# Kernel optimization log

Hardware: AMD Instinct MI355X
Metric: run time of the kernel (lower is better)

The kernel has to match this reference:

```python
import jax, jax.numpy as jnp
import numpy as np

N_NODES = 50000
N_EDGES = 800000
H = 128   # hidden_dim
E = 64    # edge_dim
LN_EPS = 1e-5


def _layer_norm(x, g, b):
    m = jnp.mean(x, axis=-1, keepdims=True)
    v = jnp.mean(jnp.square(x - m), axis=-1, keepdims=True)
    return (x - m) * jax.lax.rsqrt(v + LN_EPS) * g + b


def _gelu(x):
    return jax.nn.gelu(x, approximate=False)  # torch default exact GELU


def setup_inputs() -> dict:
    key = jax.random.key(0)
    ks = jax.random.split(key, 24)

    def lin(k, fin, fout):
        kw, kb = jax.random.split(k)
        s = 1.0 / np.sqrt(fin)
        W = jax.random.uniform(kw, (fin, fout), jnp.float32, -s, s)
        b = jax.random.uniform(kb, (fout,), jnp.float32, -s, s)
        return W, b

    inp = {}
    inp["x"] = jax.random.normal(ks[0], (N_NODES, H), jnp.float32)
    inp["edge_emb"] = jax.random.normal(ks[1], (N_EDGES, E), jnp.float32)
    inp["time_weight"] = jax.random.uniform(ks[2], (N_EDGES, 1), jnp.float32)
    inp["message_node_scale"] = jax.random.uniform(ks[3], (N_NODES, 1), jnp.float32)
    inp["ln1_g"] = jnp.ones((H,), jnp.float32)
    inp["ln1_b"] = jnp.zeros((H,), jnp.float32)
    inp["ln2_g"] = jnp.ones((H,), jnp.float32)
    inp["ln2_b"] = jnp.zeros((H,), jnp.float32)
    inp["selfW"], inp["selfb"] = lin(ks[4], H, H)
    inp["msgW1"], inp["msgb1"] = lin(ks[5], H + E, H)
    inp["msgW2"], inp["msgb2"] = lin(ks[6], H, H)
    inp["gateW1"], inp["gateb1"] = lin(ks[7], 2 * H + E, H)
    inp["gateW2"], inp["gateb2"] = lin(ks[8], H, 1)
    inp["aggW"], inp["aggb"] = lin(ks[9], H, H)
    inp["ffnW1"], inp["ffnb1"] = lin(ks[10], H, 2 * H)
    inp["ffnW2"], inp["ffnb2"] = lin(ks[11], 2 * H, H)
    inp["edge_src"] = jax.random.randint(ks[12], (N_EDGES,), 0, N_NODES, jnp.int32)
    inp["edge_dst"] = jax.random.randint(ks[13], (N_EDGES,), 0, N_NODES, jnp.int32)
    return inp


def reference(x, edge_emb, time_weight, message_node_scale,
              ln1_g, ln1_b, ln2_g, ln2_b,
              selfW, selfb, msgW1, msgb1, msgW2, msgb2,
              gateW1, gateb1, gateW2, gateb2,
              aggW, aggb, ffnW1, ffnb1, ffnW2, ffnb2,
              edge_src, edge_dst):
    n_nodes = x.shape[0]
    n_edges = edge_dst.shape[0]

    h = _layer_norm(x, ln1_g, ln1_b)
    hs = h[edge_src]  # [NE, H]
    hd = h[edge_dst]  # [NE, H]

    msg = _gelu(jnp.concatenate([hs, edge_emb], -1) @ msgW1 + msgb1) @ msgW2 + msgb2
    gate = jax.nn.sigmoid(
        _gelu(jnp.concatenate([hd, hs, edge_emb], -1) @ gateW1 + gateb1) @ gateW2 + gateb2)
    edge_repr = gate * msg
    edge_repr = edge_repr * time_weight
    edge_scale = 0.5 * (message_node_scale[edge_src] + message_node_scale[edge_dst])
    edge_repr = edge_repr * edge_scale

    agg = jax.ops.segment_sum(edge_repr, edge_dst, num_segments=n_nodes)
    deg = jax.ops.segment_sum(jnp.ones((n_edges, 1), x.dtype), edge_dst,
                              num_segments=n_nodes)
    agg = agg / jnp.maximum(deg, 1.0)

    update = (h @ selfW + selfb) + (agg @ aggW + aggb)
    out = x + update  # residual; dropout is identity at inference

    h2 = _layer_norm(out, ln2_g, ln2_b)
    ffn_update = _gelu(h2 @ ffnW1 + ffnb1) @ ffnW2 + ffnb2
    out = out + ffn_update
    return (out, edge_repr)
```

## Files before the change

### kernel.cpp

```cpp
#include <hip/hip_runtime.h>


typedef __attribute__((ext_vector_type(8))) short short8;
typedef __attribute__((ext_vector_type(4))) float f32x4;

#define NN 50000
#define NEDGE 800000

#define MFMA(a, b, c) __builtin_amdgcn_mfma_f32_16x16x32_bf16(a, b, c, 0, 0, 0)

__device__ __forceinline__ unsigned short f2bf(float f) {
  unsigned int u = __float_as_uint(f);
  u += 0x7fffu + ((u >> 16) & 1u);
  return (unsigned short)(u >> 16);
}
__device__ __forceinline__ float bf2f(unsigned short u) {
  return __uint_as_float((unsigned int)u << 16);
}
__device__ __forceinline__ unsigned int cvtpk(float a, float b) {
  unsigned int d;
  asm("v_cvt_pk_bf16_f32 %0, %1, %2" : "=v"(d) : "v"(a), "v"(b));
  return d;
}
__device__ __forceinline__ float geluf(float x) {
  const float t = x * fmaf(-0.1029437f, x * x, -2.3022211f);
  return x * __builtin_amdgcn_rcpf(1.0f + exp2f(t));
}
__device__ __forceinline__ short8 ld8(const unsigned short* p) {
  return *reinterpret_cast<const short8*>(p);
}
__device__ __forceinline__ int swz256(int row, int byteoff) {
  return row * 256 + (byteoff ^ ((row & 15) << 4));
}
__device__ __forceinline__ int swz128(int row, int byteoff) {
  return row * 128 + (byteoff ^ ((row & 7) << 4));
}

__device__ __forceinline__ void ln_frags(const float* __restrict__ rowp,
                                         const float* __restrict__ g,
                                         const float* __restrict__ b, int koff,
                                         short8 a[4]) {
  f32x4 v[8];
#pragma unroll
  for (int s = 0; s < 4; s++) {
    v[2 * s] = *reinterpret_cast<const f32x4*>(rowp + s * 32 + koff);
    v[2 * s + 1] = *reinterpret_cast<const f32x4*>(rowp + s * 32 + koff + 4);
  }
  float sm = 0.f;
#pragma unroll
  for (int i = 0; i < 8; i++) sm += v[i][0] + v[i][1] + v[i][2] + v[i][3];
  sm += __shfl_xor(sm, 16);
  sm += __shfl_xor(sm, 32);
  const float mean = sm * 0.0078125f;
  float sq = 0.f;
#pragma unroll
  for (int i = 0; i < 8; i++) {
#pragma unroll
    for (int t = 0; t < 4; t++) {
      const float d = v[i][t] - mean;
      sq += d * d;
    }
  }
  sq += __shfl_xor(sq, 16);
  sq += __shfl_xor(sq, 32);
  const float rs = rsqrtf(sq * 0.0078125f + 1e-5f);
#pragma unroll
  for (int s = 0; s < 4; s++) {
    const f32x4 glo = *reinterpret_cast<const f32x4*>(g + s * 32 + koff);
    const f32x4 ghi = *reinterpret_cast<const f32x4*>(g + s * 32 + koff + 4);
    const f32x4 blo = *reinterpret_cast<const f32x4*>(b + s * 32 + koff);
    const f32x4 bhi = *reinterpret_cast<const f32x4*>(b + s * 32 + koff + 4);
    float y[8];
#pragma unroll
    for (int t = 0; t < 4; t++) {
      y[t] = (v[2 * s][t] - mean) * rs * glo[t] + blo[t];
      y[4 + t] = (v[2 * s + 1][t] - mean) * rs * ghi[t] + bhi[t];
    }
    union { unsigned int u[4]; short8 s8; } pk;
    pk.u[0] = cvtpk(y[0], y[1]);
    pk.u[1] = cvtpk(y[2], y[3]);
    pk.u[2] = cvtpk(y[4], y[5]);
    pk.u[3] = cvtpk(y[6], y[7]);
    a[s] = pk.s8;
  }
}

__global__ __launch_bounds__(256) void prep_kernel(
    const float* __restrict__ selfW, const float* __restrict__ msgW1,
    const float* __restrict__ msgW2, const float* __restrict__ gateW1,
    const float* __restrict__ aggW, const float* __restrict__ ffnW1,
    const float* __restrict__ ffnW2, unsigned short* __restrict__ wts) {
  const int idx = blockIdx.x * 256 + threadIdx.x;
  if (idx < 16384) {
    int n = idx >> 7, k = idx & 127;
    wts[idx] = f2bf(selfW[k * 128 + n]);
  } else if (idx < 32768) {
    int l = idx - 16384, n = l >> 7, k = l & 127;
    wts[idx] = f2bf(aggW[k * 128 + n]);
  } else if (idx < 57344) {
    int l = idx - 32768, n = l / 192, k = l - n * 192;
    wts[idx] = f2bf(msgW1[k * 128 + n]);
  } else if (idx < 73728) {
    int l = idx - 57344, n = l >> 7, k = l & 127;
    wts[idx] = f2bf(msgW2[k * 128 + n]);
  } else if (idx < 114688) {
    int l = idx - 73728, n = l / 320, k = l - n * 320;
    wts[idx] = f2bf(gateW1[k * 128 + n]);
  } else if (idx < 147456) {
    int l = idx - 114688, n = l >> 7, k = l & 127;
    wts[idx] = f2bf(ffnW1[k * 256 + n]);
  } else if (idx < 180224) {
    int l = idx - 147456, n = l >> 8, k = l & 255;
    wts[idx] = f2bf(ffnW2[k * 128 + n]);
  }
}

__global__ __launch_bounds__(256) void node_pre_kernel(
    const float* __restrict__ x, const float* __restrict__ ln1g,
    const float* __restrict__ ln1b, const unsigned short* __restrict__ wts,
    unsigned short* __restrict__ pd, unsigned short* __restrict__ psm) {
  const int wid = threadIdx.x >> 6, lane = threadIdx.x & 63;
  const int q = lane >> 4, r16 = lane & 15, koff = q * 8;
  const int r0 = blockIdx.x * 64 + wid * 16;
  const int row = min(r0 + r16, NN - 1);
  const unsigned short* gateW1T = wts + 73728;
  const unsigned short* msgW1T = wts + 32768;
  short8 a[4];
  ln_frags(x + (size_t)row * 128, ln1g, ln1b, koff, a);
  f32x4 acc[3][8];
#pragma unroll
  for (int t = 0; t < 3; t++)
#pragma unroll
    for (int nt = 0; nt < 8; nt++) acc[t][nt] = (f32x4){0.f, 0.f, 0.f, 0.f};
#pragma unroll
  for (int s = 0; s < 4; s++) {
    const int k0 = s * 32 + koff;
#pragma unroll
    for (int nt = 0; nt < 8; nt++) {
      const int c = nt * 16 + r16;
      acc[0][nt] = MFMA(a[s], ld8(gateW1T + c * 320 + k0), acc[0][nt]);
      acc[1][nt] = MFMA(a[s], ld8(gateW1T + c * 320 + 128 + k0), acc[1][nt]);
      acc[2][nt] = MFMA(a[s], ld8(msgW1T + c * 192 + k0), acc[2][nt]);
    }
  }
#pragma unroll
  for (int j = 0; j < 4; j++) {
    const int gr = r0 + q * 4 + j;
    if (gr < NN) {
#pragma unroll
      for (int nt = 0; nt < 8; nt++) {
        const int c = nt * 16 + r16;
        pd[(size_t)gr * 128 + c] = f2bf(acc[0][nt][j]);
        psm[(size_t)gr * 256 + c] = f2bf(acc[1][nt][j]);
        psm[(size_t)gr * 256 + 128 + c] = f2bf(acc[2][nt][j]);
      }
    }
  }
}

__global__ __launch_bounds__(256) void count_kernel(
    const int* __restrict__ edst, int* __restrict__ cnt) {
  const int e = blockIdx.x * 256 + threadIdx.x;
  atomicAdd(&cnt[edst[e]], 1);
}

__global__ __launch_bounds__(256) void scan_sums_kernel(
    const int* __restrict__ cnt, int* __restrict__ bsum) {
  const int gi = blockIdx.x * 256 + threadIdx.x;
  int v = (gi < NN) ? cnt[gi] : 0;
#pragma unroll
  for (int m = 1; m < 64; m <<= 1) v += __shfl_xor(v, m);
  __shared__ int wsum[4];
  if ((threadIdx.x & 63) == 0) wsum[threadIdx.x >> 6] = v;
  __syncthreads();
  if (threadIdx.x == 0)
    bsum[blockIdx.x] = wsum[0] + wsum[1] + wsum[2] + wsum[3];
}

__global__ __launch_bounds__(256) void scan_offsets_kernel(
    const int* __restrict__ bsum, int* __restrict__ boff, int nb) {
  __shared__ int tmp[256];
  const int tid = threadIdx.x;
  const int v = (tid < nb) ? bsum[tid] : 0;
  tmp[tid] = v;
  __syncthreads();
#pragma unroll
  for (int d = 1; d < 256; d <<= 1) {
    const int t = (tid >= d) ? tmp[tid - d] : 0;
    __syncthreads();
    tmp[tid] += t;
    __syncthreads();
  }
  if (tid < nb) boff[tid] = tmp[tid] - v;
}

__global__ __launch_bounds__(256) void scan_final_kernel(
    const int* __restrict__ cnt, const int* __restrict__ boff,
    int* __restrict__ row_start, int* __restrict__ cursor) {
  const int tid = threadIdx.x, lane = tid & 63, wid = tid >> 6;
  const int gi = blockIdx.x * 256 + tid;
  const int val = (gi < NN) ? cnt[gi] : 0;
  int v = val;
#pragma unroll
  for (int d = 1; d < 64; d <<= 1) {
    const int t = __shfl_up(v, d);
    if (lane >= d) v += t;
  }
  __shared__ int wsum[4];
  if (lane == 63) wsum[wid] = v;
  __syncthreads();
  int woff = 0;
  for (int w = 0; w < wid; ++w) woff += wsum[w];
  const int excl = (v - val) + woff + boff[blockIdx.x];
  if (gi < NN) {
    row_start[gi] = excl;
    cursor[gi] = excl;
  }
  if (gi == NN - 1) row_start[NN] = excl + val;
}

__global__ __launch_bounds__(256) void scatter_kernel(
    const int* __restrict__ esrc, const int* __restrict__ edst,
    const float* __restrict__ tw, const float* __restrict__ mns,
    int* __restrict__ cursor, int4* __restrict__ etab) {
  const int e = blockIdx.x * 256 + threadIdx.x;
  const int si = esrc[e];
  const int di = edst[e];
  const int pos = atomicAdd(&cursor[di], 1);
  const float sc = tw[e] * 0.5f * (mns[si] + mns[di]);
  int4 v;
  v.x = e;
  v.y = si;
  v.z = di;
  v.w = __float_as_int(sc);
  etab[pos] = v;
}

__global__ __launch_bounds__(512, 6) void edge_kernel(
    const float* __restrict__ emb, const int4* __restrict__ etab,
    const unsigned short* __restrict__ pd,
    const unsigned short* __restrict__ psm,
    const unsigned short* __restrict__ wts, const float* __restrict__ msgb1,
    const float* __restrict__ msgb2, const float* __restrict__ gateb1,
    const float* __restrict__ gateW2, const float* __restrict__ gateb2v,
    float* __restrict__ erout, float* __restrict__ aggf) {
  __shared__ __align__(16) char buf[64 * 256 + 64 * 256 + 64 * 128];
  __shared__ float p_s[4][64];
  __shared__ float G_s[64];
  __shared__ float sc_s[64];
  __shared__ int di_s[64], eidx_s[64];

  char* pgp = buf;
  char* pmp = buf + 16384;
  char* embp = buf + 32768;
  float* xbuf = (float*)buf;

  const int tid = threadIdx.x;
  const int lane = tid & 63;
  const int wid = tid >> 6;
  const int q = lane >> 4;
  const int r16 = lane & 15;
  const int koff = q * 8;
  const int mg = wid >> 2;
  const int ng = wid & 3;
  const int e0 = blockIdx.x * 64;

  const unsigned short* gateW1T = wts + 73728;
  const unsigned short* msgW1T = wts + 32768;
  const unsigned short* msgW2T = wts + 57344;

  if (tid < 64) {
    const int4 et = etab[e0 + tid];
    eidx_s[tid] = et.x;
    di_s[tid] = et.z;
    sc_s[tid] = __int_as_float(et.w);
  }

#pragma unroll
  for (int r = 0; r < 2; r++) {
    const int unit = tid + 512 * r;
    const int row = unit >> 4;
    const int c = unit & 15;
    const int4 et = etab[e0 + row];
    const int si = et.y, di = et.z;
    const short8 vd = ld8(pd + (size_t)di * 128 + c * 8);
    const short8 vs = ld8(psm + (size_t)si * 256 + c * 8);
    union { unsigned int u[4]; short8 s; } pk;
#pragma unroll
    for (int h = 0; h < 4; h++) {
      const float f0 =
          bf2f((unsigned short)vd[2 * h]) + bf2f((unsigned short)vs[2 * h]);
      const float f1 = bf2f((unsigned short)vd[2 * h + 1]) +
                       bf2f((unsigned short)vs[2 * h + 1]);
      pk.u[h] = cvtpk(f0, f1);
    }
    *reinterpret_cast<short8*>(pgp + swz256(row, c * 16)) = pk.s;
    *reinterpret_cast<short8*>(pmp + swz256(row, c * 16)) =
        ld8(psm + (size_t)si * 256 + 128 + c * 8);
  }
  if (tid < 256) {
    const int row = tid >> 2, c4 = tid & 3;
    const int e = etab[e0 + row].x;
#pragma unroll
    for (int i = 0; i < 4; i++) {
      const f32x4 v =
          *reinterpret_cast<const f32x4*>(emb + (size_t)e * 64 + c4 * 16 + i * 4);
      uint2 w;
      w.x = cvtpk(v[0], v[1]);
      w.y = cvtpk(v[2], v[3]);
      *reinterpret_cast<uint2*>(embp + swz128(row, c4 * 32 + i * 8)) = w;
    }
  }
  __syncthreads();

  int cc[2];
  float g1[2], w2[2], b1m[2], b2m[2];
#pragma unroll
  for (int i = 0; i < 2; i++) {
    cc[i] = ng * 32 + i * 16 + r16;
    g1[i] = gateb1[cc[i]];
    w2[i] = gateW2[cc[i]];
    b1m[i] = msgb1[cc[i]];
    b2m[i] = msgb2[cc[i]];
  }

  f32x4 accg[2][2], acc1[2][2];
#pragma unroll
  for (int m = 0; m < 2; m++)
#pragma unroll
    for (int i = 0; i < 2; i++) {
      accg[m][i] = (f32x4){0.f, 0.f, 0.f, 0.f};
      acc1[m][i] = (f32x4){0.f, 0.f, 0.f, 0.f};
    }
#pragma unroll
  for (int s = 0; s < 2; s++) {
    const int k0 = s * 32 + koff;
    short8 a[2];
#pragma unroll
    for (int m = 0; m < 2; m++)
      a[m] = *reinterpret_cast<const short8*>(
          embp + swz128(mg * 32 + m * 16 + r16, k0 * 2));
#pragma unroll
    for (int i = 0; i < 2; i++) {
      const short8 bg = ld8(gateW1T + cc[i] * 320 + 256 + k0);
      const short8 bm = ld8(msgW1T + cc[i] * 192 + 128 + k0);
#pragma unroll
      for (int m = 0; m < 2; m++) {
        accg[m][i] = MFMA(a[m], bg, accg[m][i]);
        acc1[m][i] = MFMA(a[m], bm, acc1[m][i]);
      }
    }
  }

#pragma unroll
  for (int m = 0; m < 2; m++) {
#pragma unroll
    for (int j = 0; j < 4; j++) {
      const int row = mg * 32 + m * 16 + q * 4 + j;
      float v = 0.f;
#pragma unroll
      for (int i = 0; i < 2; i++) {
        const float pg = bf2f(*reinterpret_cast<const unsigned short*>(
            pgp + swz256(row, cc[i] * 2)));
        v += geluf(accg[m][i][j] + pg + g1[i]) * w2[i];
      }
      v += __shfl_xor(v, 1);
      v += __shfl_xor(v, 2);
      v += __shfl_xor(v, 4);
      v += __shfl_xor(v, 8);
      if (r16 == 0) p_s[ng][row] = v;
    }
  }

#pragma unroll
  for (int m = 0; m < 2; m++) {
#pragma unroll
    for (int i = 0; i < 2; i++) {
#pragma unroll
      for (int j = 0; j < 4; j++) {
        const int row = mg * 32 + m * 16 + q * 4 + j;
        unsigned short* ap =
            reinterpret_cast<unsigned short*>(pmp + swz256(row, cc[i] * 2));
        const float pm = bf2f(*ap);
        *ap = f2bf(geluf(acc1[m][i][j] + pm + b1m[i]));
      }
    }
  }
  __syncthreads();

  if (tid < 64) {
    const float p = gateb2v[0] + p_s[0][tid] + p_s[1][tid] + p_s[2][tid] +
                    p_s[3][tid];
    G_s[tid] =
        sc_s[tid] * __builtin_amdgcn_rcpf(1.f + exp2f(-1.4426950f * p));
  }

  f32x4 acc2[2][2];
#pragma unroll
  for (int m = 0; m < 2; m++)
#pragma unroll
    for (int i = 0; i < 2; i++) acc2[m][i] = (f32x4){0.f, 0.f, 0.f, 0.f};
#pragma unroll
  for (int s = 0; s < 4; s++) {
    const int k0 = s * 32 + koff;
    short8 a[2];
#pragma unroll
    for (int m = 0; m < 2; m++)
      a[m] = *reinterpret_cast<const short8*>(
          pmp + swz256(mg * 32 + m * 16 + r16, k0 * 2));
#pragma unroll
    for (int i = 0; i < 2; i++) {
      const short8 b = ld8(msgW2T + cc[i] * 128 + k0);
#pragma unroll
      for (int m = 0; m < 2; m++) acc2[m][i] = MFMA(a[m], b, acc2[m][i]);
    }
  }
  __syncthreads();

#pragma unroll
  for (int m = 0; m < 2; m++)
#pragma unroll
    for (int i = 0; i < 2; i++)
#pragma unroll
      for (int j = 0; j < 4; j++) {
        const int row = mg * 32 + m * 16 + q * 4 + j;
        xbuf[row * 132 + cc[i]] = G_s[row] * (acc2[m][i][j] + b2m[i]);
      }
  __syncthreads();

#pragma unroll
  for (int u = 0; u < 4; u++) {
    const int unit = tid + u * 512;
    const int r = unit >> 5;
    const int f4 = unit & 31;
    const f32x4 val = *reinterpret_cast<const f32x4*>(&xbuf[r * 132 + f4 * 4]);
    *reinterpret_cast<f32x4*>(erout + (size_t)eidx_s[r] * 128 + f4 * 4) = val;
  }

  {
    const int col = tid & 127;
    const int qt = tid >> 7;
    const int rbeg = qt * 16, rend = rbeg + 16;
    float acc = 0.f;
    int prev = di_s[rbeg];
    for (int r = rbeg; r < rend; ++r) {
      const int d = di_s[r];
      if (d != prev) {
        atomicAdd(&aggf[(size_t)prev * 128 + col], acc);
        acc = 0.f;
        prev = d;
      }
      acc += xbuf[r * 132 + col];
    }
    atomicAdd(&aggf[(size_t)prev * 128 + col], acc);
  }
}

__global__ __launch_bounds__(256) void node1_kernel(
    const float* __restrict__ x, const float* __restrict__ ln1g,
    const float* __restrict__ ln1b, const float* __restrict__ aggf,
    const int* __restrict__ row_start, const unsigned short* __restrict__ wts,
    const float* __restrict__ selfb, const float* __restrict__ aggb,
    float* __restrict__ out1) {
  const int wid = threadIdx.x >> 6, lane = threadIdx.x & 63;
  const int q = lane >> 4, r16 = lane & 15, koff = q * 8;
  const int r0 = blockIdx.x * 64 + wid * 16;
  const int row = min(r0 + r16, NN - 1);
  const float inv = __builtin_amdgcn_rcpf(
      fmaxf((float)(row_start[row + 1] - row_start[row]), 1.0f));
  const unsigned short* selfWT = wts;
  const unsigned short* aggWT = wts + 16384;
  short8 a1[4];
  ln_frags(x + (size_t)row * 128, ln1g, ln1b, koff, a1);
  f32x4 acc[8];
#pragma unroll
  for (int nt = 0; nt < 8; nt++) acc[nt] = (f32x4){0.f, 0.f, 0.f, 0.f};
#pragma unroll
  for (int s = 0; s < 4; s++) {
    const int k0 = s * 32 + koff;
    const float* ap = aggf + (size_t)row * 128 + k0;
    const f32x4 f0 = *reinterpret_cast<const f32x4*>(ap);
    const f32x4 f1 = *reinterpret_cast<const f32x4*>(ap + 4);
    union { unsigned int u[4]; short8 s; } pk;
    pk.u[0] = cvtpk(f0[0] * inv, f0[1] * inv);
    pk.u[1] = cvtpk(f0[2] * inv, f0[3] * inv);
    pk.u[2] = cvtpk(f1[0] * inv, f1[1] * inv);
    pk.u[3] = cvtpk(f1[2] * inv, f1[3] * inv);
#pragma unroll
    for (int nt = 0; nt < 8; nt++) {
      acc[nt] = MFMA(a1[s], ld8(selfWT + (nt * 16 + r16) * 128 + k0), acc[nt]);
      acc[nt] = MFMA(pk.s, ld8(aggWT + (nt * 16 + r16) * 128 + k0), acc[nt]);
    }
  }
#pragma unroll
  for (int j = 0; j < 4; j++) {
    const int gr = r0 + q * 4 + j;
    if (gr < NN) {
#pragma unroll
      for (int nt = 0; nt < 8; nt++) {
        const int c = r16 + 16 * nt;
        out1[(size_t)gr * 128 + c] =
            x[(size_t)gr * 128 + c] + acc[nt][j] + selfb[c] + aggb[c];
      }
    }
  }
}

__global__ __launch_bounds__(256) void ffn_kernel(
    const float* __restrict__ out1, const float* __restrict__ ln2g,
    const float* __restrict__ ln2b, const unsigned short* __restrict__ wts,
    const float* __restrict__ b1, const float* __restrict__ b2,
    float* __restrict__ outp) {
  __shared__ unsigned short ts[4][16 * 264];
  const int wid = threadIdx.x >> 6, lane = threadIdx.x & 63;
  const int q = lane >> 4, r16 = lane & 15, koff = q * 8;
  const int r0 = blockIdx.x * 64 + wid * 16;
  const int row = min(r0 + r16, NN - 1);
  const unsigned short* W1T = wts + 114688;
  const unsigned short* W2T = wts + 147456;
  short8 a[4];
  ln_frags(out1 + (size_t)row * 128, ln2g, ln2b, koff, a);
  f32x4 acc1[16];
#pragma unroll
  for (int nt = 0; nt < 16; nt++) acc1[nt] = (f32x4){0.f, 0.f, 0.f, 0.f};
#pragma unroll
  for (int s = 0; s < 4; s++) {
    const int k0 = s * 32 + koff;
#pragma unroll
    for (int nt = 0; nt < 16; nt++)
      acc1[nt] = MFMA(a[s], ld8(W1T + (nt * 16 + r16) * 128 + k0), acc1[nt]);
  }
  unsigned short* tw_ = ts[wid];
#pragma unroll
  for (int nt = 0; nt < 16; nt++) {
    const int c = r16 + 16 * nt;
    const float bb = b1[c];
#pragma unroll
    for (int j = 0; j < 4; j++)
      tw_[(q * 4 + j) * 264 + c] = f2bf(geluf(acc1[nt][j] + bb));
  }
  __syncthreads();
  f32x4 acc2[8];
#pragma unroll
  for (int nt = 0; nt < 8; nt++) acc2[nt] = (f32x4){0.f, 0.f, 0.f, 0.f};
#pragma unroll
  for (int s = 0; s < 8; s++) {
    const int k0 = s * 32 + koff;
    const short8 av = *reinterpret_cast<const short8*>(tw_ + r16 * 264 + k0);
#pragma unroll
    for (int nt = 0; nt < 8; nt++)
      acc2[nt] = MFMA(av, ld8(W2T + (nt * 16 + r16) * 256 + k0), acc2[nt]);
  }
#pragma unroll
  for (int j = 0; j < 4; j++) {
    const int gr = r0 + q * 4 + j;
    if (gr < NN) {
#pragma unroll
      for (int nt = 0; nt < 8; nt++) {
        const int c = r16 + 16 * nt;
        outp[(size_t)gr * 128 + c] =
            out1[(size_t)gr * 128 + c] + acc2[nt][j] + b2[c];
      }
    }
  }
}

extern "C" void kernel_launch(void* const* d_in, const int* in_sizes, int n_in,
                              void* d_out, int out_size, void* d_ws,
                              size_t ws_size, hipStream_t stream) {
  (void)in_sizes; (void)n_in; (void)out_size; (void)ws_size;
  const float* x = (const float*)d_in[0];
  const float* emb = (const float*)d_in[1];
  const float* tw = (const float*)d_in[2];
  const float* mns = (const float*)d_in[3];
  const float* ln1g = (const float*)d_in[4];
  const float* ln1b = (const float*)d_in[5];
  const float* ln2g = (const float*)d_in[6];
  const float* ln2b = (const float*)d_in[7];
  const float* selfW = (const float*)d_in[8];
  const float* selfb = (const float*)d_in[9];
  const float* msgW1 = (const float*)d_in[10];
  const float* msgb1 = (const float*)d_in[11];
  const float* msgW2 = (const float*)d_in[12];
  const float* msgb2 = (const float*)d_in[13];
  const float* gateW1 = (const float*)d_in[14];
  const float* gateb1 = (const float*)d_in[15];
  const float* gateW2 = (const float*)d_in[16];
  const float* gateb2 = (const float*)d_in[17];
  const float* aggW = (const float*)d_in[18];
  const float* aggb = (const float*)d_in[19];
  const float* ffnW1 = (const float*)d_in[20];
  const float* ffnb1 = (const float*)d_in[21];
  const float* ffnW2 = (const float*)d_in[22];
  const float* ffnb2 = (const float*)d_in[23];
  const int* esrc = (const int*)d_in[24];
  const int* edst = (const int*)d_in[25];

  char* ws = (char*)d_ws;
  unsigned short* pdb = (unsigned short*)(ws);
  unsigned short* psmb = (unsigned short*)(ws + 25600000);
  float* out1 = (float*)(ws + 51200000);
  unsigned short* wts = (unsigned short*)(ws + 76800000);
  int* cnt = (int*)(ws + 77160448);
  int* row_start = (int*)(ws + 77360640);
  int* cursor = (int*)(ws + 77560832);
  int* bsum = (int*)(ws + 77761024);
  int* boff = (int*)(ws + 77762048);
  int4* etab = (int4*)(ws + 77763072);

  float* out_nodes = (float*)d_out;
  float* out_edges = out_nodes + (size_t)NN * 128;
  float* aggf = out_nodes;

  const int NB_SCAN = (NN + 255) / 256;

  prep_kernel<<<704, 256, 0, stream>>>(selfW, msgW1, msgW2, gateW1, aggW,
                                       ffnW1, ffnW2, wts);
  node_pre_kernel<<<782, 256, 0, stream>>>(x, ln1g, ln1b, wts, pdb, psmb);
  hipMemsetAsync(cnt, 0, 200192, stream);
  hipMemsetAsync(aggf, 0, (size_t)NN * 128 * 4, stream);
  count_kernel<<<3125, 256, 0, stream>>>(edst, cnt);
  scan_sums_kernel<<<NB_SCAN, 256, 0, stream>>>(cnt, bsum);
  scan_offsets_kernel<<<1, 256, 0, stream>>>(bsum, boff, NB_SCAN);
  scan_final_kernel<<<NB_SCAN, 256, 0, stream>>>(cnt, boff, row_start, cursor);
  scatter_kernel<<<3125, 256, 0, stream>>>(esrc, edst, tw, mns, cursor, etab);
  edge_kernel<<<12500, 512, 0, stream>>>(emb, etab, pdb, psmb, wts, msgb1,
                                         msgb2, gateb1, gateW2, gateb2,
                                         out_edges, aggf);
  node1_kernel<<<782, 256, 0, stream>>>(x, ln1g, ln1b, aggf, row_start, wts,
                                        selfb, aggb, out1);
  ffn_kernel<<<782, 256, 0, stream>>>(out1, ln2g, ln2b, wts, ffnb1, ffnb2,
                                      out_nodes);
}
```

Baseline: 658.7 us.

## Fold memsets into kernels, add identity-MFMA partial sums, spread embedding load

Removes the two hipMemsetAsync calls by zeroing the count array inside prep_kernel and the aggregation buffer inside node_pre_kernel. In the edge kernel, the per-node precomputed partials are added to the accumulators with MFMA against an identity B matrix, replacing scalar LDS reads per element. The embedding staging is spread across all 512 threads instead of 256, and bf16 conversion uses the hardware pack instruction. These cut launch overhead and LDS/ALU work, at the cost of extra MFMA issues and the pack instruction's rounding behaviour.

Result: no change. 648.1 us (-1.6%).

```diff
diff --git a/kernel.cpp b/kernel.cpp
--- a/kernel.cpp
+++ b/kernel.cpp
@@ -21,6 +21,9 @@
   unsigned int d;
   asm("v_cvt_pk_bf16_f32 %0, %1, %2" : "=v"(d) : "v"(a), "v"(b));
   return d;
+}
+__device__ __forceinline__ unsigned short f2bf1(float a) {
+  return (unsigned short)cvtpk(a, a);
 }
 __device__ __forceinline__ float geluf(float x) {
   const float t = x * fmaf(-0.1029437f, x * x, -2.3022211f);
@@ -89,8 +92,10 @@
     const float* __restrict__ selfW, const float* __restrict__ msgW1,
     const float* __restrict__ msgW2, const float* __restrict__ gateW1,
     const float* __restrict__ aggW, const float* __restrict__ ffnW1,
-    const float* __restrict__ ffnW2, unsigned short* __restrict__ wts) {
+    const float* __restrict__ ffnW2, unsigned short* __restrict__ wts,
+    int* __restrict__ cnt) {
   const int idx = blockIdx.x * 256 + threadIdx.x;
+  if (idx <= NN) cnt[idx] = 0;
   if (idx < 16384) {
     int n = idx >> 7, k = idx & 127;
     wts[idx] = f2bf(selfW[k * 128 + n]);
@@ -118,11 +123,21 @@
 __global__ __launch_bounds__(256) void node_pre_kernel(
     const float* __restrict__ x, const float* __restrict__ ln1g,
     const float* __restrict__ ln1b, const unsigned short* __restrict__ wts,
-    unsigned short* __restrict__ pd, unsigned short* __restrict__ psm) {
+    unsigned short* __restrict__ pd, unsigned short* __restrict__ psm,
+    float* __restrict__ aggf) {
   const int wid = threadIdx.x >> 6, lane = threadIdx.x & 63;
   const int q = lane >> 4, r16 = lane & 15, koff = q * 8;
   const int r0 = blockIdx.x * 64 + wid * 16;
   const int row = min(r0 + r16, NN - 1);
+  {
+    const int t = blockIdx.x * 256 + threadIdx.x;
+    const f32x4 z = (f32x4){0.f, 0.f, 0.f, 0.f};
+#pragma unroll
+    for (int k = 0; k < 8; k++) {
+      const int pos = t + k * 200192;
+      if (pos < NN * 32) reinterpret_cast<f32x4*>(aggf)[pos] = z;
+    }
+  }
   const unsigned short* gateW1T = wts + 73728;
   const unsigned short* msgW1T = wts + 32768;
   short8 a[4];
@@ -298,18 +313,18 @@
     *reinterpret_cast<short8*>(pmp + swz256(row, c * 16)) =
         ld8(psm + (size_t)si * 256 + 128 + c * 8);
   }
-  if (tid < 256) {
-    const int row = tid >> 2, c4 = tid & 3;
+#pragma unroll
+  for (int r = 0; r < 2; r++) {
+    const int unit = tid + 512 * r;
+    const int row = unit >> 4;
+    const int c4 = unit & 15;
     const int e = etab[e0 + row].x;
-#pragma unroll
-    for (int i = 0; i < 4; i++) {
-      const f32x4 v =
-          *reinterpret_cast<const f32x4*>(emb + (size_t)e * 64 + c4 * 16 + i * 4);
-      uint2 w;
-      w.x = cvtpk(v[0], v[1]);
-      w.y = cvtpk(v[2], v[3]);
-      *reinterpret_cast<uint2*>(embp + swz128(row, c4 * 32 + i * 8)) = w;
-    }
+    const f32x4 v =
+        *reinterpret_cast<const f32x4*>(emb + (size_t)e * 64 + c4 * 4);
+    uint2 w;
+    w.x = cvtpk(v[0], v[1]);
+    w.y = cvtpk(v[2], v[3]);
+    *reinterpret_cast<uint2*>(embp + swz128(row, c4 * 8)) = w;
   }
   __syncthreads();
 
@@ -324,6 +339,14 @@
     b2m[i] = msgb2[cc[i]];
   }
 
+  short8 bI[2];
+#pragma unroll
+  for (int h = 0; h < 8; h++) {
+    const int kk = koff + h;
+    bI[0][h] = (kk == r16) ? (short)0x3F80 : (short)0;
+    bI[1][h] = (kk == r16 + 16) ? (short)0x3F80 : (short)0;
+  }
+
   f32x4 accg[2][2], acc1[2][2];
 #pragma unroll
   for (int m = 0; m < 2; m++)
@@ -352,18 +375,30 @@
     }
   }
 
+  {
+    const int kw = ng * 32 + koff;
+#pragma unroll
+    for (int m = 0; m < 2; m++) {
+      const int row = mg * 32 + m * 16 + r16;
+      const short8 apg =
+          *reinterpret_cast<const short8*>(pgp + swz256(row, kw * 2));
+      const short8 apm =
+          *reinterpret_cast<const short8*>(pmp + swz256(row, kw * 2));
+#pragma unroll
+      for (int i = 0; i < 2; i++) {
+        accg[m][i] = MFMA(apg, bI[i], accg[m][i]);
+        acc1[m][i] = MFMA(apm, bI[i], acc1[m][i]);
+      }
+    }
+  }
+
 #pragma unroll
   for (int m = 0; m < 2; m++) {
 #pragma unroll
     for (int j = 0; j < 4; j++) {
       const int row = mg * 32 + m * 16 + q * 4 + j;
-      float v = 0.f;
-#pragma unroll
-      for (int i = 0; i < 2; i++) {
-        const float pg = bf2f(*reinterpret_cast<const unsigned short*>(
-            pgp + swz256(row, cc[i] * 2)));
-        v += geluf(accg[m][i][j] + pg + g1[i]) * w2[i];
-      }
+      float v = geluf(accg[m][0][j] + g1[0]) * w2[0] +
+                geluf(accg[m][1][j] + g1[1]) * w2[1];
       v += __shfl_xor(v, 1);
       v += __shfl_xor(v, 2);
       v += __shfl_xor(v, 4);
@@ -379,10 +414,8 @@
 #pragma unroll
       for (int j = 0; j < 4; j++) {
         const int row = mg * 32 + m * 16 + q * 4 + j;
-        unsigned short* ap =
-            reinterpret_cast<unsigned short*>(pmp + swz256(row, cc[i] * 2));
-        const float pm = bf2f(*ap);
-        *ap = f2bf(geluf(acc1[m][i][j] + pm + b1m[i]));
+        *reinterpret_cast<unsigned short*>(pmp + swz256(row, cc[i] * 2)) =
+            f2bf1(geluf(acc1[m][i][j] + b1m[i]));
       }
     }
   }
@@ -537,7 +570,7 @@
     const float bb = b1[c];
 #pragma unroll
     for (int j = 0; j < 4; j++)
-      tw_[(q * 4 + j) * 264 + c] = f2bf(geluf(acc1[nt][j] + bb));
+      tw_[(q * 4 + j) * 264 + c] = f2bf1(geluf(acc1[nt][j] + bb));
   }
   __syncthreads();
   f32x4 acc2[8];
@@ -615,10 +648,9 @@
   const int NB_SCAN = (NN + 255) / 256;
 
   prep_kernel<<<704, 256, 0, stream>>>(selfW, msgW1, msgW2, gateW1, aggW,
-                                       ffnW1, ffnW2, wts);
-  node_pre_kernel<<<782, 256, 0, stream>>>(x, ln1g, ln1b, wts, pdb, psmb);
-  hipMemsetAsync(cnt, 0, 200192, stream);
-  hipMemsetAsync(aggf, 0, (size_t)NN * 128 * 4, stream);
+                                       ffnW1, ffnW2, wts, cnt);
+  node_pre_kernel<<<782, 256, 0, stream>>>(x, ln1g, ln1b, wts, pdb, psmb,
+                                           aggf);
   count_kernel<<<3125, 256, 0, stream>>>(edst, cnt);
   scan_sums_kernel<<<NB_SCAN, 256, 0, stream>>>(cnt, bsum);
   scan_offsets_kernel<<<1, 256, 0, stream>>>(bsum, boff, NB_SCAN);
```
